# Kernel optimization log

Measured on AMD Instinct MI355X. Metric: run time of the kernel, lower is better.

## Reference

```python
import jax, jax.numpy as jnp
import numpy as np

N, E, IN, HID, OUT = 100000, 1600000, 128, 64, 64
NEG = 0.2   # GATConv negative_slope default
EPS = 1e-5


def _gat(x, src, dst, W, a_s, a_d, b, n):
    # PyG GATConv, heads=1: h = x W; e_ij = LeakyReLU(a_s.h_j + a_d.h_i);
    # softmax over incoming edges of i; out_i = sum_j alpha_ij h_j + b
    h = x @ W                                   # [N, F]
    s = (h @ a_s)[src] + (h @ a_d)[dst]         # [E]
    e = jnp.where(s >= 0, s, NEG * s)
    m = jax.ops.segment_max(e, dst, num_segments=n)
    w = jnp.exp(e - m[dst])
    z = jax.ops.segment_sum(w, dst, num_segments=n)
    alpha = w / z[dst]
    out = jax.ops.segment_sum(h[src] * alpha[:, None], dst, num_segments=n)
    return out + b


def _graph_ln(x, g, b):
    # PyG LayerNorm mode='graph' (default): normalize over all nodes+features
    mu = jnp.mean(x)
    var = jnp.mean((x - mu) ** 2)
    return (x - mu) * jax.lax.rsqrt(var + EPS) * g + b


def _prelu(x, a):
    return jnp.where(x >= 0, x, a * x)


def _encoder(x, edge_index, params):
    n = x.shape[0]
    loops = jnp.arange(n, dtype=edge_index.dtype)  # GATConv add_self_loops=True
    src = jnp.concatenate([edge_index[0], loops])
    dst = jnp.concatenate([edge_index[1], loops])
    for (W, a_s, a_d, b, g, be, p) in params:
        x = _gat(x, src, dst, W, a_s, a_d, b, n)
        x = _graph_ln(x, g, be)
        x = _prelu(x, p)
    return x


def setup_inputs():
    key = jax.random.key(0)
    ks = jax.random.split(key, 32)
    d = {}
    d["x_q"] = jax.random.normal(ks[0], (N, IN), jnp.float32)
    d["x_k"] = jax.random.normal(ks[1], (N, IN), jnp.float32)
    d["edge_index_q"] = jax.random.randint(ks[2], (2, E), 0, N)
    d["edge_index_k"] = jax.random.randint(ks[3], (2, E), 0, N)
    i = 4
    for pre, fi, fo in [("q1", IN, HID), ("q2", HID, OUT), ("k1", IN, HID), ("k2", HID, OUT)]:
        d[pre + "_W"] = jax.random.normal(ks[i], (fi, fo), jnp.float32) / np.sqrt(fi).astype(np.float32); i += 1
        d[pre + "_as"] = jax.random.normal(ks[i], (fo,), jnp.float32) * 0.1; i += 1
        d[pre + "_ad"] = jax.random.normal(ks[i], (fo,), jnp.float32) * 0.1; i += 1
        d[pre + "_b"] = jnp.zeros((fo,), jnp.float32)
        d[pre + "_g"] = jnp.ones((fo,), jnp.float32)
        d[pre + "_be"] = jnp.zeros((fo,), jnp.float32)
        d[pre + "_p"] = jnp.full((1,), 0.25, jnp.float32)
    d["m_W1"] = jax.random.normal(ks[i], (OUT, 2 * OUT), jnp.float32) / np.sqrt(OUT).astype(np.float32); i += 1
    d["m_b1"] = jnp.zeros((2 * OUT,), jnp.float32)
    d["m_p"] = jnp.full((1,), 0.25, jnp.float32)
    d["m_W2"] = jax.random.normal(ks[i], (2 * OUT, OUT), jnp.float32) / np.sqrt(2 * OUT).astype(np.float32)
    d["m_b2"] = jnp.zeros((OUT,), jnp.float32)
    return d


def reference(x_q, x_k, edge_index_q, edge_index_k,
              q1_W, q1_as, q1_ad, q1_b, q1_g, q1_be, q1_p,
              q2_W, q2_as, q2_ad, q2_b, q2_g, q2_be, q2_p,
              k1_W, k1_as, k1_ad, k1_b, k1_g, k1_be, k1_p,
              k2_W, k2_as, k2_ad, k2_b, k2_g, k2_be, k2_p,
              m_W1, m_b1, m_p, m_W2, m_b2):
    Q = _encoder(x_q, edge_index_q,
                 [(q1_W, q1_as, q1_ad, q1_b, q1_g, q1_be, q1_p),
                  (q2_W, q2_as, q2_ad, q2_b, q2_g, q2_be, q2_p)])
    Q = _prelu(Q @ m_W1 + m_b1, m_p) @ m_W2 + m_b2
    K = _encoder(x_k, edge_index_k,
                 [(k1_W, k1_as, k1_ad, k1_b, k1_g, k1_be, k1_p),
                  (k2_W, k2_as, k2_ad, k2_b, k2_g, k2_be, k2_p)])
    return (Q, jax.lax.stop_gradient(K))
```

## Files before the change

### kernel.cpp

```cpp
#include <hip/hip_runtime.h>
#include <cstddef>
#include <cstdint>

#define NEG_SLOPE 0.2f
#define LN_EPS    1e-5f
#define NBUK      256
#define MAXNPB    512

typedef unsigned short ushort_t;
typedef short bf16x8 __attribute__((ext_vector_type(8)));
typedef float f32x4  __attribute__((ext_vector_type(4)));

__device__ __forceinline__ float lrelu(float s) { return s >= 0.f ? s : NEG_SLOPE * s; }
__device__ __forceinline__ float b2f(ushort_t u) { return __uint_as_float(((uint32_t)u) << 16); }
__device__ __forceinline__ ushort_t f2b(float f) {
  uint32_t u = __float_as_uint(f);
  return (ushort_t)((u + 0x7fffu + ((u >> 16) & 1u)) >> 16);
}
__device__ __forceinline__ uint2 pack4(float4 v) {
  uint2 r;
  r.x = (uint32_t)f2b(v.x) | ((uint32_t)f2b(v.y) << 16);
  r.y = (uint32_t)f2b(v.z) | ((uint32_t)f2b(v.w) << 16);
  return r;
}


__global__ void kb_init(int* __restrict__ gbcur, int cap) {
  gbcur[threadIdx.x] = threadIdx.x * cap;
}

__global__ __launch_bounds__(256) void kb_expand(const int* __restrict__ src,
                                                 const int* __restrict__ dst, int E,
                                                 int* __restrict__ gbcur,
                                                 int2* __restrict__ pairs, uint32_t bmul) {
  __shared__ int hist[NBUK], base[NBUK], lcnt[NBUK];
  const int tid = threadIdx.x;
  const int nchunk = (E + 4095) >> 12;
  for (int c = blockIdx.x; c < nchunk; c += gridDim.x) {
    const int e0 = c << 12;
    hist[tid] = 0; lcnt[tid] = 0;
    __syncthreads();
    int sv[16], dv[16], bv[16];
    #pragma unroll
    for (int u = 0; u < 16; ++u) {
      const int i = e0 + u * 256 + tid;
      if (i < E) {
        sv[u] = src[i]; dv[u] = dst[i];
        bv[u] = (int)__umulhi((uint32_t)dv[u], bmul);
        atomicAdd(&hist[bv[u]], 1);
      } else bv[u] = -1;
    }
    __syncthreads();
    base[tid] = atomicAdd(&gbcur[tid], hist[tid]);
    __syncthreads();
    #pragma unroll
    for (int u = 0; u < 16; ++u) {
      if (bv[u] >= 0) {
        const int pos = atomicAdd(&lcnt[bv[u]], 1);
        pairs[base[bv[u]] + pos] = make_int2(sv[u], dv[u]);
      }
    }
    __syncthreads();
  }
}

__global__ __launch_bounds__(256) void kb_sort(const int2* __restrict__ pairs,
                                               const int* __restrict__ gbcur,
                                               int* __restrict__ rs, int* __restrict__ re,
                                               int* __restrict__ csr,
                                               uint32_t bmul, int cap, int N) {
  __shared__ int hist[MAXNPB];
  __shared__ int ps[256];
  const int b = blockIdx.x, tid = threadIdx.x;
  int n0 = (int)((((uint64_t)b << 32) + bmul - 1) / bmul);
  int n1 = (int)((((uint64_t)(b + 1) << 32) + bmul - 1) / bmul);
  n0 = n0 < N ? n0 : N;
  n1 = n1 < N ? n1 : N;
  const int nn = n1 - n0;
  const int e0 = b * cap;
  const int e1 = min(gbcur[b], e0 + cap);
  for (int k = tid; k < nn; k += 256) hist[k] = 0;
  __syncthreads();
  for (int i = e0 + tid; i < e1; i += 256) atomicAdd(&hist[pairs[i].y - n0], 1);
  __syncthreads();
  const int i0 = 2 * tid, i1 = 2 * tid + 1;
  const int a = (i0 < nn) ? hist[i0] : 0;
  const int c = (i1 < nn) ? hist[i1] : 0;
  const int tot = a + c;
  ps[tid] = tot;
  __syncthreads();
  for (int off = 1; off < 256; off <<= 1) {
    const int x = (tid >= off) ? ps[tid - off] : 0;
    __syncthreads();
    ps[tid] += x;
    __syncthreads();
  }
  const int excl = ps[tid] - tot;
  if (i0 < nn) { hist[i0] = excl;     rs[n0 + i0] = e0 + excl;     re[n0 + i0] = e0 + excl + a; }
  if (i1 < nn) { hist[i1] = excl + a; rs[n0 + i1] = e0 + excl + a; re[n0 + i1] = e0 + excl + a + c; }
  __syncthreads();
  for (int i = e0 + tid; i < e1; i += 256) {
    const int2 e = pairs[i];
    const int p = atomicAdd(&hist[e.y - n0], 1);
    csr[e0 + p] = e.x;
  }
}

template <int FI, bool LNF>
__global__ __launch_bounds__(256) void k_gemm_att(
    const void* __restrict__ act, int N,
    const float* __restrict__ W, const float* __restrict__ a_s, const float* __restrict__ a_d,
    const float* __restrict__ stats, const float* __restrict__ g,
    const float* __restrict__ be, const float* __restrict__ pp,
    ushort_t* __restrict__ h16, float* __restrict__ hs, float* __restrict__ hd)
{
  constexpr int P = FI + 8;
  __shared__ ushort_t S[64 * P];
  const int tid = threadIdx.x, wid = tid >> 6, lane = tid & 63;
  const int l15 = lane & 15, lhi = lane >> 4;

  for (int idx = tid; idx < FI * 64; idx += 256) {
    const int k = idx >> 6, f = idx & 63;
    S[f * P + k] = f2b(W[idx]);
  }
  __syncthreads();
  bf16x8 Bf[FI / 32][4];
  #pragma unroll
  for (int kt = 0; kt < FI / 32; ++kt)
    #pragma unroll
    for (int nt = 0; nt < 4; ++nt)
      Bf[kt][nt] = *(const bf16x8*)&S[(nt * 16 + l15) * P + kt * 32 + lhi * 8];
  __syncthreads();

  float asf[4], adf[4];
  #pragma unroll
  for (int nt = 0; nt < 4; ++nt) { asf[nt] = a_s[nt * 16 + l15]; adf[nt] = a_d[nt * 16 + l15]; }
  float mu = 0.f, rstd = 1.f, p0 = 0.f;
  if (LNF) { mu = stats[0]; rstd = stats[1]; p0 = pp[0]; }

  const int ntiles = (N + 63) >> 6;
  for (int tile = blockIdx.x; tile < ntiles; tile += gridDim.x) {
    const int nb = tile << 6;
    {
      const int r = tid >> 2;
      const int node = nb + r;
      if (node < N) {
        if (LNF) {
          const ushort_t* a16 = (const ushort_t*)act;
          const int q = tid & 3;
          const int4* srcp = (const int4*)(a16 + (size_t)node * 64 + q * 16);
          const int4 A0 = srcp[0], A1 = srcp[1];
          const ushort_t* pu0 = (const ushort_t*)&A0;
          const ushort_t* pu1 = (const ushort_t*)&A1;
          float vv[16];
          #pragma unroll
          for (int i = 0; i < 8; ++i) { vv[i] = b2f(pu0[i]); vv[8 + i] = b2f(pu1[i]); }
          #pragma unroll
          for (int i2 = 0; i2 < 4; ++i2) {
            const int c4 = q * 4 + i2;
            const float4 gg = ((const float4*)g)[c4];
            const float4 bb = ((const float4*)be)[c4];
            float4 v;
            v.x = (vv[i2 * 4 + 0] - mu) * rstd * gg.x + bb.x;  v.x = v.x >= 0.f ? v.x : p0 * v.x;
            v.y = (vv[i2 * 4 + 1] - mu) * rstd * gg.y + bb.y;  v.y = v.y >= 0.f ? v.y : p0 * v.y;
            v.z = (vv[i2 * 4 + 2] - mu) * rstd * gg.z + bb.z;  v.z = v.z >= 0.f ? v.z : p0 * v.z;
            v.w = (vv[i2 * 4 + 3] - mu) * rstd * gg.w + bb.w;  v.w = v.w >= 0.f ? v.w : p0 * v.w;
            *(uint2*)&S[r * P + c4 * 4] = pack4(v);
          }
        } else {
          const float4* srcp = (const float4*)((const float*)act + (size_t)node * FI);
          #pragma unroll
          for (int i = 0; i < FI / 16; ++i) {
            const int c = (tid & 3) * (FI / 4) + i * 4;
            const float4 v = srcp[c >> 2];
            *(uint2*)&S[r * P + c] = pack4(v);
          }
        }
      }
    }
    __syncthreads();

    const f32x4 fz = {0.f, 0.f, 0.f, 0.f};
    f32x4 acc[4]; acc[0] = fz; acc[1] = fz; acc[2] = fz; acc[3] = fz;
    #pragma unroll
    for (int kt = 0; kt < FI / 32; ++kt) {
      const bf16x8 Af = *(const bf16x8*)&S[(wid * 16 + l15) * P + kt * 32 + lhi * 8];
      #pragma unroll
      for (int nt = 0; nt < 4; ++nt)
        acc[nt] = __builtin_amdgcn_mfma_f32_16x16x32_bf16(Af, Bf[kt][nt], acc[nt], 0, 0, 0);
    }
    #pragma unroll
    for (int r = 0; r < 4; ++r) {
      float ps = acc[0][r] * asf[0] + acc[1][r] * asf[1] + acc[2][r] * asf[2] + acc[3][r] * asf[3];
      float pd = acc[0][r] * adf[0] + acc[1][r] * adf[1] + acc[2][r] * adf[2] + acc[3][r] * adf[3];
      #pragma unroll
      for (int off = 1; off < 16; off <<= 1) { ps += __shfl_xor(ps, off); pd += __shfl_xor(pd, off); }
      const int node = nb + wid * 16 + lhi * 4 + r;
      if (l15 == 0 && node < N) { hs[node] = ps; hd[node] = pd; }
    }
    #pragma unroll
    for (int nt = 0; nt < 4; ++nt)
      #pragma unroll
      for (int r = 0; r < 4; ++r)
        S[(wid * 16 + lhi * 4 + r) * P + nt * 16 + l15] = f2b(acc[nt][r]);
    __syncthreads();
    {
      const int r = tid >> 2, chunk = tid & 3;
      const int node = nb + r;
      if (node < N) {
        const int4* sp = (const int4*)&S[r * P + chunk * 16];
        const int4 v0 = sp[0], v1 = sp[1];
        int4* dp = (int4*)(h16 + (size_t)node * 64 + chunk * 16);
        dp[0] = v0; dp[1] = v1;
      }
    }
    __syncthreads();
  }
}

__global__ __launch_bounds__(256) void k_aggregate(
    const int* __restrict__ rs, const int* __restrict__ re, const int* __restrict__ csr,
    const ushort_t* __restrict__ h16, const float* __restrict__ hs, const float* __restrict__ hd,
    const float* __restrict__ bias, int N,
    ushort_t* __restrict__ y16, float* __restrict__ part)
{
  __shared__ float wsh[4][32];
  __shared__ float sh1[4], sh2[4];
  const int tid = threadIdx.x, wid = tid >> 6, lane = tid & 63;
  const int node = blockIdx.x * 4 + wid;
  float val = 0.f;
  if (node < N) {
    const float hdi = hd[node];
    const float wself = __expf(lrelu(hs[node] + hdi));
    float z = wself;
    float acc0 = wself * b2f(h16[((size_t)(uint32_t)node << 6) + lane]);
    float acc1 = 0.f, acc2 = 0.f, acc3 = 0.f;
    const int st = __builtin_amdgcn_readfirstlane(rs[node]);
    const int en = __builtin_amdgcn_readfirstlane(re[node]);
    for (int j = st; j < en; j += 32) {
      const int m = min(32, en - j);
      int sA = 0;
      if (lane < m) sA = csr[j + lane];
      #define GA(u) h16[((size_t)(uint32_t)__builtin_amdgcn_readlane(sA, u) << 6) + lane]
      ushort_t g0 = 0, g1 = 0, g2 = 0, g3 = 0, g4 = 0, g5 = 0, g6 = 0, g7 = 0;
      ushort_t g8 = 0, g9 = 0, g10 = 0, g11 = 0, g12 = 0, g13 = 0, g14 = 0, g15 = 0;
      ushort_t g16 = 0, g17 = 0, g18 = 0, g19 = 0, g20 = 0, g21 = 0, g22 = 0, g23 = 0;
      ushort_t g24 = 0, g25 = 0, g26 = 0, g27 = 0, g28 = 0, g29 = 0, g30 = 0, g31 = 0;
      if (m > 0)  { g0  = GA(0);  g1  = GA(1);  g2  = GA(2);  g3  = GA(3);  }
      if (m > 4)  { g4  = GA(4);  g5  = GA(5);  g6  = GA(6);  g7  = GA(7);  }
      if (m > 8)  { g8  = GA(8);  g9  = GA(9);  g10 = GA(10); g11 = GA(11); }
      if (m > 12) { g12 = GA(12); g13 = GA(13); g14 = GA(14); g15 = GA(15); }
      if (m > 16) { g16 = GA(16); g17 = GA(17); g18 = GA(18); g19 = GA(19); }
      if (m > 20) { g20 = GA(20); g21 = GA(21); g22 = GA(22); g23 = GA(23); }
      if (m > 24) { g24 = GA(24); g25 = GA(25); g26 = GA(26); g27 = GA(27); }
      if (m > 28) { g28 = GA(28); g29 = GA(29); g30 = GA(30); g31 = GA(31); }
      #undef GA
      float wA = 0.f;
      if (lane < m) wA = __expf(lrelu(hs[sA] + hdi));
      if (lane < 32) wsh[wid][lane] = wA;
      float ws = wA;
      #pragma unroll
      for (int off = 32; off; off >>= 1) ws += __shfl_xor(ws, off);
      z += ws;
      #define CS(u, a) a = fmaf(wsh[wid][u], b2f(g##u), a)
      if (m > 0)  { CS(0, acc0);  CS(1, acc1);  CS(2, acc2);  CS(3, acc3);  }
      if (m > 4)  { CS(4, acc0);  CS(5, acc1);  CS(6, acc2);  CS(7, acc3);  }
      if (m > 8)  { CS(8, acc0);  CS(9, acc1);  CS(10, acc2); CS(11, acc3); }
      if (m > 12) { CS(12, acc0); CS(13, acc1); CS(14, acc2); CS(15, acc3); }
      if (m > 16) { CS(16, acc0); CS(17, acc1); CS(18, acc2); CS(19, acc3); }
      if (m > 20) { CS(20, acc0); CS(21, acc1); CS(22, acc2); CS(23, acc3); }
      if (m > 24) { CS(24, acc0); CS(25, acc1); CS(26, acc2); CS(27, acc3); }
      if (m > 28) { CS(28, acc0); CS(29, acc1); CS(30, acc2); CS(31, acc3); }
      #undef CS
    }
    val = ((acc0 + acc1) + (acc2 + acc3)) / z + bias[lane];
    y16[(size_t)node * 64 + lane] = f2b(val);
  }
  float s1r = val, s2r = val * val;
  #pragma unroll
  for (int off = 32; off; off >>= 1) { s1r += __shfl_xor(s1r, off); s2r += __shfl_xor(s2r, off); }
  if (lane == 0) { sh1[wid] = s1r; sh2[wid] = s2r; }
  __syncthreads();
  if (tid == 0) {
    part[(size_t)blockIdx.x * 2 + 0] = sh1[0] + sh1[1] + sh1[2] + sh1[3];
    part[(size_t)blockIdx.x * 2 + 1] = sh2[0] + sh2[1] + sh2[2] + sh2[3];
  }
}

__global__ __launch_bounds__(1024) void k_ln_stats(
    const float* __restrict__ part, int nblk, float invCount, float* __restrict__ statsOut)
{
  __shared__ float sh1[16], sh2[16];
  float s1 = 0.f, s2 = 0.f;
  for (int i = threadIdx.x; i < nblk; i += 1024) { s1 += part[(size_t)i * 2]; s2 += part[(size_t)i * 2 + 1]; }
  #pragma unroll
  for (int off = 32; off; off >>= 1) { s1 += __shfl_xor(s1, off); s2 += __shfl_xor(s2, off); }
  const int wid = threadIdx.x >> 6, lane = threadIdx.x & 63;
  if (lane == 0) { sh1[wid] = s1; sh2[wid] = s2; }
  __syncthreads();
  if (threadIdx.x == 0) {
    float t1 = 0.f, t2 = 0.f;
    #pragma unroll
    for (int i = 0; i < 16; ++i) { t1 += sh1[i]; t2 += sh2[i]; }
    const float mu = t1 * invCount;
    const float var = t2 * invCount - mu * mu;
    statsOut[0] = mu;
    statsOut[1] = rsqrtf(var + LN_EPS);
  }
}

__global__ __launch_bounds__(256) void k_mlp(
    const ushort_t* __restrict__ y16, int N,
    const float* __restrict__ stats, const float* __restrict__ g,
    const float* __restrict__ be, const float* __restrict__ pe,
    const float* __restrict__ W1, const float* __restrict__ b1, const float* __restrict__ pm,
    const float* __restrict__ W2, const float* __restrict__ b2,
    float* __restrict__ outp)
{
  __shared__ ushort_t W1t[128 * 72];
  __shared__ ushort_t W2t[64 * 136];
  __shared__ ushort_t At[64 * 72];
  __shared__ ushort_t Tt[64 * 136];
  __shared__ float    Ob[64 * 68];
  const int tid = threadIdx.x, wid = tid >> 6, lane = tid & 63;
  const int l15 = lane & 15, lhi = lane >> 4;

  for (int idx = tid; idx < 64 * 128; idx += 256) {
    const int k = idx >> 7, f = idx & 127;
    W1t[f * 72 + k] = f2b(W1[idx]);
  }
  for (int idx = tid; idx < 128 * 64; idx += 256) {
    const int k = idx >> 6, f = idx & 63;
    W2t[f * 136 + k] = f2b(W2[idx]);
  }
  __syncthreads();

  const float mu = stats[0], rstd = stats[1], p0 = pe[0], pm0 = pm[0];
  float b1f[8], b2f_[4];
  #pragma unroll
  for (int nt = 0; nt < 8; ++nt) b1f[nt] = b1[nt * 16 + l15];
  #pragma unroll
  for (int nt = 0; nt < 4; ++nt) b2f_[nt] = b2[nt * 16 + l15];

  const int ntiles = (N + 63) >> 6;
  for (int tile = blockIdx.x; tile < ntiles; tile += gridDim.x) {
    const int nb = tile << 6;
    {
      const int r = tid >> 2;
      const int node = nb + r;
      if (node < N) {
        const int q = tid & 3;
        const int4* srcp = (const int4*)(y16 + (size_t)node * 64 + q * 16);
        const int4 A0 = srcp[0], A1 = srcp[1];
        const ushort_t* pu0 = (const ushort_t*)&A0;
        const ushort_t* pu1 = (const ushort_t*)&A1;
        float vv[16];
        #pragma unroll
        for (int i = 0; i < 8; ++i) { vv[i] = b2f(pu0[i]); vv[8 + i] = b2f(pu1[i]); }
        #pragma unroll
        for (int i2 = 0; i2 < 4; ++i2) {
          const int c4 = q * 4 + i2;
          const float4 gg = ((const float4*)g)[c4];
          const float4 bb = ((const float4*)be)[c4];
          float4 v;
          v.x = (vv[i2 * 4 + 0] - mu) * rstd * gg.x + bb.x;  v.x = v.x >= 0.f ? v.x : p0 * v.x;
          v.y = (vv[i2 * 4 + 1] - mu) * rstd * gg.y + bb.y;  v.y = v.y >= 0.f ? v.y : p0 * v.y;
          v.z = (vv[i2 * 4 + 2] - mu) * rstd * gg.z + bb.z;  v.z = v.z >= 0.f ? v.z : p0 * v.z;
          v.w = (vv[i2 * 4 + 3] - mu) * rstd * gg.w + bb.w;  v.w = v.w >= 0.f ? v.w : p0 * v.w;
          *(uint2*)&At[r * 72 + c4 * 4] = pack4(v);
        }
      }
    }
    __syncthreads();

    const f32x4 fz = {0.f, 0.f, 0.f, 0.f};
    f32x4 acc1[8];
    #pragma unroll
    for (int nt = 0; nt < 8; ++nt) acc1[nt] = fz;
    #pragma unroll
    for (int kt = 0; kt < 2; ++kt) {
      const bf16x8 Af = *(const bf16x8*)&At[(wid * 16 + l15) * 72 + kt * 32 + lhi * 8];
      #pragma unroll
      for (int nt = 0; nt < 8; ++nt) {
        const bf16x8 Bf = *(const bf16x8*)&W1t[(nt * 16 + l15) * 72 + kt * 32 + lhi * 8];
        acc1[nt] = __builtin_amdgcn_mfma_f32_16x16x32_bf16(Af, Bf, acc1[nt], 0, 0, 0);
      }
    }
    #pragma unroll
    for (int nt = 0; nt < 8; ++nt)
      #pragma unroll
      for (int r = 0; r < 4; ++r) {
        float v = acc1[nt][r] + b1f[nt];
        v = v >= 0.f ? v : pm0 * v;
        Tt[(wid * 16 + lhi * 4 + r) * 136 + nt * 16 + l15] = f2b(v);
      }
    __syncthreads();

    f32x4 acc2[4];
    #pragma unroll
    for (int nt = 0; nt < 4; ++nt) acc2[nt] = fz;
    #pragma unroll
    for (int kt = 0; kt < 4; ++kt) {
      const bf16x8 Af = *(const bf16x8*)&Tt[(wid * 16 + l15) * 136 + kt * 32 + lhi * 8];
      #pragma unroll
      for (int nt = 0; nt < 4; ++nt) {
        const bf16x8 Bf = *(const bf16x8*)&W2t[(nt * 16 + l15) * 136 + kt * 32 + lhi * 8];
        acc2[nt] = __builtin_amdgcn_mfma_f32_16x16x32_bf16(Af, Bf, acc2[nt], 0, 0, 0);
      }
    }
    #pragma unroll
    for (int nt = 0; nt < 4; ++nt)
      #pragma unroll
      for (int r = 0; r < 4; ++r)
        Ob[(wid * 16 + lhi * 4 + r) * 68 + nt * 16 + l15] = acc2[nt][r] + b2f_[nt];
    __syncthreads();
    {
      const int r = tid >> 2, chunk = tid & 3;
      const int node = nb + r;
      if (node < N) {
        const float4* sp = (const float4*)&Ob[r * 68 + chunk * 16];
        const float4 v0 = sp[0], v1 = sp[1], v2 = sp[2], v3 = sp[3];
        float4* dp = (float4*)(outp + (size_t)node * 64 + chunk * 16);
        dp[0] = v0; dp[1] = v1; dp[2] = v2; dp[3] = v3;
      }
    }
    __syncthreads();
  }
}

__global__ void k_ln_prelu_out(const ushort_t* __restrict__ y16, int total8,
                               const float* __restrict__ stats, const float* __restrict__ g,
                               const float* __restrict__ be, const float* __restrict__ pe,
                               float* __restrict__ o)
{
  const float mu = stats[0], rstd = stats[1], p0 = pe[0];
  int i = blockIdx.x * blockDim.x + threadIdx.x;
  const int stride = gridDim.x * blockDim.x;
  for (; i < total8; i += stride) {
    const int4 A = *(const int4*)(y16 + (size_t)i * 8);
    const ushort_t* pu = (const ushort_t*)&A;
    const int grp = i & 7;
    const float4 g0 = ((const float4*)g)[grp * 2], g1 = ((const float4*)g)[grp * 2 + 1];
    const float4 b0 = ((const float4*)be)[grp * 2], b1 = ((const float4*)be)[grp * 2 + 1];
    float4 o0, o1;
    o0.x = (b2f(pu[0]) - mu) * rstd * g0.x + b0.x;  o0.x = o0.x >= 0.f ? o0.x : p0 * o0.x;
    o0.y = (b2f(pu[1]) - mu) * rstd * g0.y + b0.y;  o0.y = o0.y >= 0.f ? o0.y : p0 * o0.y;
    o0.z = (b2f(pu[2]) - mu) * rstd * g0.z + b0.z;  o0.z = o0.z >= 0.f ? o0.z : p0 * o0.z;
    o0.w = (b2f(pu[3]) - mu) * rstd * g0.w + b0.w;  o0.w = o0.w >= 0.f ? o0.w : p0 * o0.w;
    o1.x = (b2f(pu[4]) - mu) * rstd * g1.x + b1.x;  o1.x = o1.x >= 0.f ? o1.x : p0 * o1.x;
    o1.y = (b2f(pu[5]) - mu) * rstd * g1.y + b1.y;  o1.y = o1.y >= 0.f ? o1.y : p0 * o1.y;
    o1.z = (b2f(pu[6]) - mu) * rstd * g1.z + b1.z;  o1.z = o1.z >= 0.f ? o1.z : p0 * o1.z;
    o1.w = (b2f(pu[7]) - mu) * rstd * g1.w + b1.w;  o1.w = o1.w >= 0.f ? o1.w : p0 * o1.w;
    float4* dp = (float4*)(o + (size_t)i * 8);
    dp[0] = o0; dp[1] = o1;
  }
}

extern "C" void kernel_launch(void* const* d_in, const int* in_sizes, int n_in,
                              void* d_out, int out_size, void* d_ws, size_t ws_size,
                              hipStream_t stream) {
  (void)n_in; (void)out_size; (void)ws_size;
  const int FIN = 128, F = 64;
  const int N = in_sizes[0] / FIN;
  const int E = in_sizes[2] / 2;

  const float* x_q = (const float*)d_in[0];
  const float* x_k = (const float*)d_in[1];
  const int*   ei_q = (const int*)d_in[2];
  const int*   ei_k = (const int*)d_in[3];
  const float* L[4][7];
  for (int l = 0; l < 4; ++l)
    for (int j = 0; j < 7; ++j) L[l][j] = (const float*)d_in[4 + l * 7 + j];
  const float* mW1 = (const float*)d_in[32];
  const float* mb1 = (const float*)d_in[33];
  const float* mp  = (const float*)d_in[34];
  const float* mW2 = (const float*)d_in[35];
  const float* mb2 = (const float*)d_in[36];
  float* out = (float*)d_out;

  const int CAP = (((E + NBUK - 1) / NBUK) * 3 / 2 + 3) & ~3;

  char* w = (char*)d_ws;
  auto alloc = [&](size_t bytes) { char* r = w; w += (bytes + 255) & ~size_t(255); return r; };
  ushort_t* h16 = (ushort_t*)alloc((size_t)N * F * sizeof(ushort_t));
  ushort_t* y16 = (ushort_t*)alloc((size_t)N * F * sizeof(ushort_t));
  float* hs    = (float*)alloc((size_t)N * sizeof(float));
  float* hd    = (float*)alloc((size_t)N * sizeof(float));
  const int nblk = (N + 3) / 4;
  float* part  = (float*)alloc((size_t)nblk * 2 * sizeof(float));
  float* stats = (float*)alloc(16 * sizeof(float));
  int* rs      = (int*)alloc((size_t)N * sizeof(int));
  int* re      = (int*)alloc((size_t)N * sizeof(int));
  int* csr     = (int*)alloc((size_t)NBUK * CAP * sizeof(int));
  int* bcur    = (int*)alloc(NBUK * sizeof(int));
  int2* pairs  = (int2*)alloc((size_t)NBUK * CAP * sizeof(int2));

  const float invCount = 1.f / ((float)N * (float)F);
  const uint32_t bmul = (uint32_t)(((uint64_t)NBUK << 32) / (uint64_t)N);

  auto build_csr = [&](const int* ei) {
    kb_init<<<1, NBUK, 0, stream>>>(bcur, CAP);
    kb_expand<<<512, 256, 0, stream>>>(ei, ei + E, E, bcur, pairs, bmul);
    kb_sort<<<NBUK, 256, 0, stream>>>(pairs, bcur, rs, re, csr, bmul, CAP, N);
  };

  auto run_layers = [&](const float* x0, int li0) {
    const float* const* A = L[li0];
    k_gemm_att<128, false><<<512, 256, 0, stream>>>(
        x0, N, A[0], A[1], A[2], nullptr, nullptr, nullptr, nullptr, h16, hs, hd);
    k_aggregate<<<nblk, 256, 0, stream>>>(rs, re, csr, h16, hs, hd, A[3], N, y16, part);
    k_ln_stats<<<1, 1024, 0, stream>>>(part, nblk, invCount, stats + 2 * li0);
    const float* const* B = L[li0 + 1];
    k_gemm_att<64, true><<<512, 256, 0, stream>>>(
        y16, N, B[0], B[1], B[2], stats + 2 * li0, A[4], A[5], A[6], h16, hs, hd);
    k_aggregate<<<nblk, 256, 0, stream>>>(rs, re, csr, h16, hs, hd, B[3], N, y16, part);
    k_ln_stats<<<1, 1024, 0, stream>>>(part, nblk, invCount, stats + 2 * (li0 + 1));
  };

  build_csr(ei_q);
  run_layers(x_q, 0);
  k_mlp<<<512, 256, 0, stream>>>(y16, N, stats + 2, L[1][4], L[1][5], L[1][6],
                                 mW1, mb1, mp, mW2, mb2, out);

  build_csr(ei_k);
  run_layers(x_k, 2);
  const int total8 = N * F / 8;
  k_ln_prelu_out<<<2048, 256, 0, stream>>>(y16, total8, stats + 6,
                                           L[3][4], L[3][5], L[3][6],
                                           out + (size_t)N * F);
}
```

Baseline: 453.7 us.

## Batch query and key encoder stages into shared dual-path kernel launches

```diff
diff --git a/kernel.cpp b/kernel.cpp
--- a/kernel.cpp
+++ b/kernel.cpp
@@ -24,54 +24,67 @@
   return r;
 }
 
-
-__global__ void kb_init(int* __restrict__ gbcur, int cap) {
-  gbcur[threadIdx.x] = threadIdx.x * cap;
-}
-
-__global__ __launch_bounds__(256) void kb_expand(const int* __restrict__ src,
-                                                 const int* __restrict__ dst, int E,
-                                                 int* __restrict__ gbcur,
-                                                 int2* __restrict__ pairs, uint32_t bmul) {
+__global__ void kb_init(int* __restrict__ b0, int* __restrict__ b1, int cap) {
+  b0[threadIdx.x] = threadIdx.x * cap;
+  b1[threadIdx.x] = threadIdx.x * cap;
+}
+
+__global__ __launch_bounds__(256) void kb_expand(
+    const int* __restrict__ ei0, const int* __restrict__ ei1, int E, int nchunk,
+    int* __restrict__ bcur0, int* __restrict__ bcur1,
+    int2* __restrict__ pairs0, int2* __restrict__ pairs1, uint32_t bmul) {
   __shared__ int hist[NBUK], base[NBUK], lcnt[NBUK];
   const int tid = threadIdx.x;
-  const int nchunk = (E + 4095) >> 12;
-  for (int c = blockIdx.x; c < nchunk; c += gridDim.x) {
-    const int e0 = c << 12;
-    hist[tid] = 0; lcnt[tid] = 0;
-    __syncthreads();
-    int sv[16], dv[16], bv[16];
-    #pragma unroll
-    for (int u = 0; u < 16; ++u) {
-      const int i = e0 + u * 256 + tid;
-      if (i < E) {
-        sv[u] = src[i]; dv[u] = dst[i];
-        bv[u] = (int)__umulhi((uint32_t)dv[u], bmul);
-        atomicAdd(&hist[bv[u]], 1);
-      } else bv[u] = -1;
-    }
-    __syncthreads();
-    base[tid] = atomicAdd(&gbcur[tid], hist[tid]);
-    __syncthreads();
-    #pragma unroll
-    for (int u = 0; u < 16; ++u) {
-      if (bv[u] >= 0) {
-        const int pos = atomicAdd(&lcnt[bv[u]], 1);
-        pairs[base[bv[u]] + pos] = make_int2(sv[u], dv[u]);
-      }
-    }
-    __syncthreads();
-  }
-}
-
-__global__ __launch_bounds__(256) void kb_sort(const int2* __restrict__ pairs,
-                                               const int* __restrict__ gbcur,
-                                               int* __restrict__ rs, int* __restrict__ re,
-                                               int* __restrict__ csr,
-                                               uint32_t bmul, int cap, int N) {
+  const int path = (blockIdx.x >= (unsigned)nchunk) ? 1 : 0;
+  const int c = blockIdx.x - path * nchunk;
+  const int* src = path ? ei1 : ei0;
+  const int* dst = src + E;
+  int* gbcur = path ? bcur1 : bcur0;
+  int2* pairs = path ? pairs1 : pairs0;
+
+  const int e0 = c << 12;
+  hist[tid] = 0; lcnt[tid] = 0;
+  __syncthreads();
+  int sv[16], dv[16], bv[16];
+  #pragma unroll
+  for (int u = 0; u < 16; ++u) {
+    const int i = e0 + u * 256 + tid;
+    if (i < E) {
+      sv[u] = src[i]; dv[u] = dst[i];
+      bv[u] = (int)__umulhi((uint32_t)dv[u], bmul);
+      atomicAdd(&hist[bv[u]], 1);
+    } else bv[u] = -1;
+  }
+  __syncthreads();
+  base[tid] = atomicAdd(&gbcur[tid], hist[tid]);
+  __syncthreads();
+  #pragma unroll
+  for (int u = 0; u < 16; ++u) {
+    if (bv[u] >= 0) {
+      const int pos = atomicAdd(&lcnt[bv[u]], 1);
+      pairs[base[bv[u]] + pos] = make_int2(sv[u], dv[u]);
+    }
+  }
+}
+
+__global__ __launch_bounds__(256) void kb_sort(
+    const int2* __restrict__ pairs0, const int2* __restrict__ pairs1,
+    const int* __restrict__ bcur0, const int* __restrict__ bcur1,
+    int* __restrict__ rs0, int* __restrict__ rs1,
+    int* __restrict__ re0, int* __restrict__ re1,
+    int* __restrict__ csr0, int* __restrict__ csr1,
+    uint32_t bmul, int cap, int N) {
   __shared__ int hist[MAXNPB];
   __shared__ int ps[256];
-  const int b = blockIdx.x, tid = threadIdx.x;
+  const int path = (blockIdx.x >= NBUK) ? 1 : 0;
+  const int b = blockIdx.x & (NBUK - 1);
+  const int tid = threadIdx.x;
+  const int2* pairs = path ? pairs1 : pairs0;
+  const int* gbcur = path ? bcur1 : bcur0;
+  int* rs = path ? rs1 : rs0;
+  int* re = path ? re1 : re0;
+  int* csr = path ? csr1 : csr0;
+
   int n0 = (int)((((uint64_t)b << 32) + bmul - 1) / bmul);
   int n1 = (int)((((uint64_t)(b + 1) << 32) + bmul - 1) / bmul);
   n0 = n0 < N ? n0 : N;
@@ -108,17 +121,37 @@
 
 template <int FI, bool LNF>
 __global__ __launch_bounds__(256) void k_gemm_att(
-    const void* __restrict__ act, int N,
-    const float* __restrict__ W, const float* __restrict__ a_s, const float* __restrict__ a_d,
-    const float* __restrict__ stats, const float* __restrict__ g,
-    const float* __restrict__ be, const float* __restrict__ pp,
-    ushort_t* __restrict__ h16, float* __restrict__ hs, float* __restrict__ hd)
+    const void* __restrict__ act0, const void* __restrict__ act1, int N, int ntiles,
+    const float* __restrict__ W0, const float* __restrict__ W1x,
+    const float* __restrict__ as0, const float* __restrict__ as1,
+    const float* __restrict__ ad0, const float* __restrict__ ad1,
+    const float* __restrict__ st0, const float* __restrict__ st1,
+    const float* __restrict__ g0, const float* __restrict__ g1,
+    const float* __restrict__ be0, const float* __restrict__ be1,
+    const float* __restrict__ pp0, const float* __restrict__ pp1,
+    ushort_t* __restrict__ h0, ushort_t* __restrict__ h1,
+    float* __restrict__ hs0, float* __restrict__ hs1,
+    float* __restrict__ hd0, float* __restrict__ hd1)
 {
   constexpr int P = FI + 8;
   __shared__ ushort_t S[64 * P];
   const int tid = threadIdx.x, wid = tid >> 6, lane = tid & 63;
   const int l15 = lane & 15, lhi = lane >> 4;
 
+  const int path = (blockIdx.x >= (unsigned)ntiles) ? 1 : 0;
+  const int tile = blockIdx.x - path * ntiles;
+  const void* act = path ? act1 : act0;
+  const float* W  = path ? W1x : W0;
+  const float* a_s = path ? as1 : as0;
+  const float* a_d = path ? ad1 : ad0;
+  const float* stats = path ? st1 : st0;
+  const float* g  = path ? g1 : g0;
+  const float* be = path ? be1 : be0;
+  const float* pp = path ? pp1 : pp0;
+  ushort_t* h16 = path ? h1 : h0;
+  float* hs = path ? hs1 : hs0;
+  float* hd = path ? hd1 : hd0;
+
   for (int idx = tid; idx < FI * 64; idx += 256) {
     const int k = idx >> 6, f = idx & 63;
     S[f * P + k] = f2b(W[idx]);
@@ -138,96 +171,110 @@
   float mu = 0.f, rstd = 1.f, p0 = 0.f;
   if (LNF) { mu = stats[0]; rstd = stats[1]; p0 = pp[0]; }
 
-  const int ntiles = (N + 63) >> 6;
-  for (int tile = blockIdx.x; tile < ntiles; tile += gridDim.x) {
-    const int nb = tile << 6;
-    {
-      const int r = tid >> 2;
-      const int node = nb + r;
-      if (node < N) {
-        if (LNF) {
-          const ushort_t* a16 = (const ushort_t*)act;
-          const int q = tid & 3;
-          const int4* srcp = (const int4*)(a16 + (size_t)node * 64 + q * 16);
-          const int4 A0 = srcp[0], A1 = srcp[1];
-          const ushort_t* pu0 = (const ushort_t*)&A0;
-          const ushort_t* pu1 = (const ushort_t*)&A1;
-          float vv[16];
-          #pragma unroll
-          for (int i = 0; i < 8; ++i) { vv[i] = b2f(pu0[i]); vv[8 + i] = b2f(pu1[i]); }
-          #pragma unroll
-          for (int i2 = 0; i2 < 4; ++i2) {
-            const int c4 = q * 4 + i2;
-            const float4 gg = ((const float4*)g)[c4];
-            const float4 bb = ((const float4*)be)[c4];
-            float4 v;
-            v.x = (vv[i2 * 4 + 0] - mu) * rstd * gg.x + bb.x;  v.x = v.x >= 0.f ? v.x : p0 * v.x;
-            v.y = (vv[i2 * 4 + 1] - mu) * rstd * gg.y + bb.y;  v.y = v.y >= 0.f ? v.y : p0 * v.y;
-            v.z = (vv[i2 * 4 + 2] - mu) * rstd * gg.z + bb.z;  v.z = v.z >= 0.f ? v.z : p0 * v.z;
-            v.w = (vv[i2 * 4 + 3] - mu) * rstd * gg.w + bb.w;  v.w = v.w >= 0.f ? v.w : p0 * v.w;
-            *(uint2*)&S[r * P + c4 * 4] = pack4(v);
-          }
-        } else {
-          const float4* srcp = (const float4*)((const float*)act + (size_t)node * FI);
-          #pragma unroll
-          for (int i = 0; i < FI / 16; ++i) {
-            const int c = (tid & 3) * (FI / 4) + i * 4;
-            const float4 v = srcp[c >> 2];
-            *(uint2*)&S[r * P + c] = pack4(v);
-          }
+  const int nb = tile << 6;
+  {
+    const int r = tid >> 2;
+    const int node = nb + r;
+    if (node < N) {
+      if (LNF) {
+        const ushort_t* a16 = (const ushort_t*)act;
+        const int q = tid & 3;
+        const int4* srcp = (const int4*)(a16 + (size_t)node * 64 + q * 16);
+        const int4 A0 = srcp[0], A1 = srcp[1];
+        const ushort_t* pu0 = (const ushort_t*)&A0;
+        const ushort_t* pu1 = (const ushort_t*)&A1;
+        float vv[16];
+        #pragma unroll
+        for (int i = 0; i < 8; ++i) { vv[i] = b2f(pu0[i]); vv[8 + i] = b2f(pu1[i]); }
+        #pragma unroll
+        for (int i2 = 0; i2 < 4; ++i2) {
+          const int c4 = q * 4 + i2;
+          const float4 gg = ((const float4*)g)[c4];
+          const float4 bb = ((const float4*)be)[c4];
+          float4 v;
+          v.x = (vv[i2 * 4 + 0] - mu) * rstd * gg.x + bb.x;  v.x = v.x >= 0.f ? v.x : p0 * v.x;
+          v.y = (vv[i2 * 4 + 1] - mu) * rstd * gg.y + bb.y;  v.y = v.y >= 0.f ? v.y : p0 * v.y;
+          v.z = (vv[i2 * 4 + 2] - mu) * rstd * gg.z + bb.z;  v.z = v.z >= 0.f ? v.z : p0 * v.z;
+          v.w = (vv[i2 * 4 + 3] - mu) * rstd * gg.w + bb.w;  v.w = v.w >= 0.f ? v.w : p0 * v.w;
+          *(uint2*)&S[r * P + c4 * 4] = pack4(v);
+        }
+      } else {
+        const float4* srcp = (const float4*)((const float*)act + (size_t)node * FI);
+        #pragma unroll
+        for (int i = 0; i < FI / 16; ++i) {
+          const int c = (tid & 3) * (FI / 4) + i * 4;
+          const float4 v = srcp[c >> 2];
+          *(uint2*)&S[r * P + c] = pack4(v);
         }
       }
     }
-    __syncthreads();
-
-    const f32x4 fz = {0.f, 0.f, 0.f, 0.f};
-    f32x4 acc[4]; acc[0] = fz; acc[1] = fz; acc[2] = fz; acc[3] = fz;
-    #pragma unroll
-    for (int kt = 0; kt < FI / 32; ++kt) {
-      const bf16x8 Af = *(const bf16x8*)&S[(wid * 16 + l15) * P + kt * 32 + lhi * 8];
-      #pragma unroll
-      for (int nt = 0; nt < 4; ++nt)
-        acc[nt] = __builtin_amdgcn_mfma_f32_16x16x32_bf16(Af, Bf[kt][nt], acc[nt], 0, 0, 0);
-    }
-    #pragma unroll
-    for (int r = 0; r < 4; ++r) {
-      float ps = acc[0][r] * asf[0] + acc[1][r] * asf[1] + acc[2][r] * asf[2] + acc[3][r] * asf[3];
-      float pd = acc[0][r] * adf[0] + acc[1][r] * adf[1] + acc[2][r] * adf[2] + acc[3][r] * adf[3];
-      #pragma unroll
-      for (int off = 1; off < 16; off <<= 1) { ps += __shfl_xor(ps, off); pd += __shfl_xor(pd, off); }
-      const int node = nb + wid * 16 + lhi * 4 + r;
-      if (l15 == 0 && node < N) { hs[node] = ps; hd[node] = pd; }
-    }
+  }
+  __syncthreads();
+
+  const f32x4 fz = {0.f, 0.f, 0.f, 0.f};
+  f32x4 acc[4]; acc[0] = fz; acc[1] = fz; acc[2] = fz; acc[3] = fz;
+  #pragma unroll
+  for (int kt = 0; kt < FI / 32; ++kt) {
+    const bf16x8 Af = *(const bf16x8*)&S[(wid * 16 + l15) * P + kt * 32 + lhi * 8];
     #pragma unroll
     for (int nt = 0; nt < 4; ++nt)
-      #pragma unroll
-      for (int r = 0; r < 4; ++r)
-        S[(wid * 16 + lhi * 4 + r) * P + nt * 16 + l15] = f2b(acc[nt][r]);
-    __syncthreads();
-    {
-      const int r = tid >> 2, chunk = tid & 3;
-      const int node = nb + r;
-      if (node < N) {
-        const int4* sp = (const int4*)&S[r * P + chunk * 16];
-        const int4 v0 = sp[0], v1 = sp[1];
-        int4* dp = (int4*)(h16 + (size_t)node * 64 + chunk * 16);
-        dp[0] = v0; dp[1] = v1;
-      }
-    }
-    __syncthreads();
+      acc[nt] = __builtin_amdgcn_mfma_f32_16x16x32_bf16(Af, Bf[kt][nt], acc[nt], 0, 0, 0);
+  }
+  #pragma unroll
+  for (int r = 0; r < 4; ++r) {
+    float ps = acc[0][r] * asf[0] + acc[1][r] * asf[1] + acc[2][r] * asf[2] + acc[3][r] * asf[3];
+    float pd = acc[0][r] * adf[0] + acc[1][r] * adf[1] + acc[2][r] * adf[2] + acc[3][r] * adf[3];
+    #pragma unroll
+    for (int off = 1; off < 16; off <<= 1) { ps += __shfl_xor(ps, off); pd += __shfl_xor(pd, off); }
+    const int node = nb + wid * 16 + lhi * 4 + r;
+    if (l15 == 0 && node < N) { hs[node] = ps; hd[node] = pd; }
+  }
+  #pragma unroll
+  for (int nt = 0; nt < 4; ++nt)
+    #pragma unroll
+    for (int r = 0; r < 4; ++r)
+      S[(wid * 16 + lhi * 4 + r) * P + nt * 16 + l15] = f2b(acc[nt][r]);
+  __syncthreads();
+  {
+    const int r = tid >> 2, chunk = tid & 3;
+    const int node = nb + r;
+    if (node < N) {
+      const int4* sp = (const int4*)&S[r * P + chunk * 16];
+      const int4 v0 = sp[0], v1 = sp[1];
+      int4* dp = (int4*)(h16 + (size_t)node * 64 + chunk * 16);
+      dp[0] = v0; dp[1] = v1;
+    }
   }
 }
 
 __global__ __launch_bounds__(256) void k_aggregate(
-    const int* __restrict__ rs, const int* __restrict__ re, const int* __restrict__ csr,
-    const ushort_t* __restrict__ h16, const float* __restrict__ hs, const float* __restrict__ hd,
-    const float* __restrict__ bias, int N,
-    ushort_t* __restrict__ y16, float* __restrict__ part)
+    const int* __restrict__ rs0, const int* __restrict__ rs1,
+    const int* __restrict__ re0, const int* __restrict__ re1,
+    const int* __restrict__ csr0, const int* __restrict__ csr1,
+    const ushort_t* __restrict__ h0, const ushort_t* __restrict__ h1,
+    const float* __restrict__ hs0, const float* __restrict__ hs1,
+    const float* __restrict__ hd0, const float* __restrict__ hd1,
+    const float* __restrict__ bias0, const float* __restrict__ bias1,
+    int N, int nblk,
+    ushort_t* __restrict__ y0, ushort_t* __restrict__ y1,
+    float* __restrict__ part0, float* __restrict__ part1)
 {
   __shared__ float wsh[4][32];
   __shared__ float sh1[4], sh2[4];
   const int tid = threadIdx.x, wid = tid >> 6, lane = tid & 63;
-  const int node = blockIdx.x * 4 + wid;
+  const int path = (blockIdx.x >= (unsigned)nblk) ? 1 : 0;
+  const int bb = blockIdx.x - path * nblk;
+  const int* rs = path ? rs1 : rs0;
+  const int* re = path ? re1 : re0;
+  const int* csr = path ? csr1 : csr0;
+  const ushort_t* h16 = path ? h1 : h0;
+  const float* hs = path ? hs1 : hs0;
+  const float* hd = path ? hd1 : hd0;
+  const float* bias = path ? bias1 : bias0;
+  ushort_t* y16 = path ? y1 : y0;
+  float* part = path ? part1 : part0;
+
+  const int node = bb * 4 + wid;
   float val = 0.f;
   if (node < N) {
     const float hdi = hd[node];
@@ -282,30 +329,33 @@
   if (lane == 0) { sh1[wid] = s1r; sh2[wid] = s2r; }
   __syncthreads();
   if (tid == 0) {
-    part[(size_t)blockIdx.x * 2 + 0] = sh1[0] + sh1[1] + sh1[2] + sh1[3];
-    part[(size_t)blockIdx.x * 2 + 1] = sh2[0] + sh2[1] + sh2[2] + sh2[3];
+    part[(size_t)bb * 2 + 0] = sh1[0] + sh1[1] + sh1[2] + sh1[3];
+    part[(size_t)bb * 2 + 1] = sh2[0] + sh2[1] + sh2[2] + sh2[3];
   }
 }
 
 __global__ __launch_bounds__(1024) void k_ln_stats(
-    const float* __restrict__ part, int nblk, float invCount, float* __restrict__ statsOut)
+    const float* __restrict__ part0, const float* __restrict__ part1,
+    int nblk, float invCount,
+    float* __restrict__ s0, float* __restrict__ s1)
 {
   __shared__ float sh1[16], sh2[16];
-  float s1 = 0.f, s2 = 0.f;
-  for (int i = threadIdx.x; i < nblk; i += 1024) { s1 += part[(size_t)i * 2]; s2 += part[(size_t)i * 2 + 1]; }
-  #pragma unroll
-  for (int off = 32; off; off >>= 1) { s1 += __shfl_xor(s1, off); s2 += __shfl_xor(s2, off); }
+  const float* part = blockIdx.x ? part1 : part0;
+  float* so = blockIdx.x ? s1 : s0;
+  float a = 0.f, b = 0.f;
+  for (int i = threadIdx.x; i < nblk; i += 1024) { a += part[(size_t)i * 2]; b += part[(size_t)i * 2 + 1]; }
+  #pragma unroll
+  for (int off = 32; off; off >>= 1) { a += __shfl_xor(a, off); b += __shfl_xor(b, off); }
   const int wid = threadIdx.x >> 6, lane = threadIdx.x & 63;
-  if (lane == 0) { sh1[wid] = s1; sh2[wid] = s2; }
+  if (lane == 0) { sh1[wid] = a; sh2[wid] = b; }
   __syncthreads();
   if (threadIdx.x == 0) {
     float t1 = 0.f, t2 = 0.f;
     #pragma unroll
     for (int i = 0; i < 16; ++i) { t1 += sh1[i]; t2 += sh2[i]; }
     const float mu = t1 * invCount;
-    const float var = t2 * invCount - mu * mu;
-    statsOut[0] = mu;
-    statsOut[1] = rsqrtf(var + LN_EPS);
+    so[0] = mu;
+    so[1] = rsqrtf(t2 * invCount - mu * mu + LN_EPS);
   }
 }
 
@@ -335,105 +385,104 @@
   }
   __syncthreads();
 
-  const float mu = stats[0], rstd = stats[1], p0 = pe[0], pm0 = pm[0];
+  const float mu = stats[0], rstd = stats[1];
+  const float p0 = pe[0], pm0 = pm[0];
   float b1f[8], b2f_[4];
   #pragma unroll
   for (int nt = 0; nt < 8; ++nt) b1f[nt] = b1[nt * 16 + l15];
   #pragma unroll
   for (int nt = 0; nt < 4; ++nt) b2f_[nt] = b2[nt * 16 + l15];
 
-  const int ntiles = (N + 63) >> 6;
-  for (int tile = blockIdx.x; tile < ntiles; tile += gridDim.x) {
-    const int nb = tile << 6;
-    {
-      const int r = tid >> 2;
-      const int node = nb + r;
-      if (node < N) {
-        const int q = tid & 3;
-        const int4* srcp = (const int4*)(y16 + (size_t)node * 64 + q * 16);
-        const int4 A0 = srcp[0], A1 = srcp[1];
-        const ushort_t* pu0 = (const ushort_t*)&A0;
-        const ushort_t* pu1 = (const ushort_t*)&A1;
-        float vv[16];
-        #pragma unroll
-        for (int i = 0; i < 8; ++i) { vv[i] = b2f(pu0[i]); vv[8 + i] = b2f(pu1[i]); }
-        #pragma unroll
-        for (int i2 = 0; i2 < 4; ++i2) {
-          const int c4 = q * 4 + i2;
-          const float4 gg = ((const float4*)g)[c4];
-          const float4 bb = ((const float4*)be)[c4];
-          float4 v;
-          v.x = (vv[i2 * 4 + 0] - mu) * rstd * gg.x + bb.x;  v.x = v.x >= 0.f ? v.x : p0 * v.x;
-          v.y = (vv[i2 * 4 + 1] - mu) * rstd * gg.y + bb.y;  v.y = v.y >= 0.f ? v.y : p0 * v.y;
-          v.z = (vv[i2 * 4 + 2] - mu) * rstd * gg.z + bb.z;  v.z = v.z >= 0.f ? v.z : p0 * v.z;
-          v.w = (vv[i2 * 4 + 3] - mu) * rstd * gg.w + bb.w;  v.w = v.w >= 0.f ? v.w : p0 * v.w;
-          *(uint2*)&At[r * 72 + c4 * 4] = pack4(v);
-        }
+  const int nb = blockIdx.x << 6;
+  {
+    const int r = tid >> 2;
+    const int node = nb + r;
+    if (node < N) {
+      const int q = tid & 3;
+      const int4* srcp = (const int4*)(y16 + (size_t)node * 64 + q * 16);
+      const int4 A0 = srcp[0], A1 = srcp[1];
+      const ushort_t* pu0 = (const ushort_t*)&A0;
+      const ushort_t* pu1 = (const ushort_t*)&A1;
+      float vv[16];
+      #pragma unroll
+      for (int i = 0; i < 8; ++i) { vv[i] = b2f(pu0[i]); vv[8 + i] = b2f(pu1[i]); }
+      #pragma unroll
+      for (int i2 = 0; i2 < 4; ++i2) {
+        const int c4 = q * 4 + i2;
+        const float4 gg = ((const float4*)g)[c4];
+        const float4 bb = ((const float4*)be)[c4];
+        float4 v;
+        v.x = (vv[i2 * 4 + 0] - mu) * rstd * gg.x + bb.x;  v.x = v.x >= 0.f ? v.x : p0 * v.x;
+        v.y = (vv[i2 * 4 + 1] - mu) * rstd * gg.y + bb.y;  v.y = v.y >= 0.f ? v.y : p0 * v.y;
+        v.z = (vv[i2 * 4 + 2] - mu) * rstd * gg.z + bb.z;  v.z = v.z >= 0.f ? v.z : p0 * v.z;
+        v.w = (vv[i2 * 4 + 3] - mu) * rstd * gg.w + bb.w;  v.w = v.w >= 0.f ? v.w : p0 * v.w;
+        *(uint2*)&At[r * 72 + c4 * 4] = pack4(v);
       }
     }
-    __syncthreads();
-
-    const f32x4 fz = {0.f, 0.f, 0.f, 0.f};
-    f32x4 acc1[8];
-    #pragma unroll
-    for (int nt = 0; nt < 8; ++nt) acc1[nt] = fz;
-    #pragma unroll
-    for (int kt = 0; kt < 2; ++kt) {
-      const bf16x8 Af = *(const bf16x8*)&At[(wid * 16 + l15) * 72 + kt * 32 + lhi * 8];
-      #pragma unroll
-      for (int nt = 0; nt < 8; ++nt) {
-        const bf16x8 Bf = *(const bf16x8*)&W1t[(nt * 16 + l15) * 72 + kt * 32 + lhi * 8];
-        acc1[nt] = __builtin_amdgcn_mfma_f32_16x16x32_bf16(Af, Bf, acc1[nt], 0, 0, 0);
-      }
-    }
-    #pragma unroll
-    for (int nt = 0; nt < 8; ++nt)
-      #pragma unroll
-      for (int r = 0; r < 4; ++r) {
-        float v = acc1[nt][r] + b1f[nt];
-        v = v >= 0.f ? v : pm0 * v;
-        Tt[(wid * 16 + lhi * 4 + r) * 136 + nt * 16 + l15] = f2b(v);
-      }
-    __syncthreads();
-
-    f32x4 acc2[4];
-    #pragma unroll
-    for (int nt = 0; nt < 4; ++nt) acc2[nt] = fz;
-    #pragma unroll
-    for (int kt = 0; kt < 4; ++kt) {
-      const bf16x8 Af = *(const bf16x8*)&Tt[(wid * 16 + l15) * 136 + kt * 32 + lhi * 8];
-      #pragma unroll
-      for (int nt = 0; nt < 4; ++nt) {
-        const bf16x8 Bf = *(const bf16x8*)&W2t[(nt * 16 + l15) * 136 + kt * 32 + lhi * 8];
-        acc2[nt] = __builtin_amdgcn_mfma_f32_16x16x32_bf16(Af, Bf, acc2[nt], 0, 0, 0);
-      }
-    }
-    #pragma unroll
-    for (int nt = 0; nt < 4; ++nt)
-      #pragma unroll
-      for (int r = 0; r < 4; ++r)
-        Ob[(wid * 16 + lhi * 4 + r) * 68 + nt * 16 + l15] = acc2[nt][r] + b2f_[nt];
-    __syncthreads();
-    {
-      const int r = tid >> 2, chunk = tid & 3;
-      const int node = nb + r;
-      if (node < N) {
-        const float4* sp = (const float4*)&Ob[r * 68 + chunk * 16];
-        const float4 v0 = sp[0], v1 = sp[1], v2 = sp[2], v3 = sp[3];
-        float4* dp = (float4*)(outp + (size_t)node * 64 + chunk * 16);
-        dp[0] = v0; dp[1] = v1; dp[2] = v2; dp[3] = v3;
-      }
-    }
-    __syncthreads();
+  }
+  __syncthreads();
+
+  const f32x4 fz = {0.f, 0.f, 0.f, 0.f};
+  f32x4 acc1[8];
+  #pragma unroll
+  for (int nt = 0; nt < 8; ++nt) acc1[nt] = fz;
+  #pragma unroll
+  for (int kt = 0; kt < 2; ++kt) {
+    const bf16x8 Af = *(const bf16x8*)&At[(wid * 16 + l15) * 72 + kt * 32 + lhi * 8];
+    #pragma unroll
+    for (int nt = 0; nt < 8; ++nt) {
+      const bf16x8 Bf = *(const bf16x8*)&W1t[(nt * 16 + l15) * 72 + kt * 32 + lhi * 8];
+      acc1[nt] = __builtin_amdgcn_mfma_f32_16x16x32_bf16(Af, Bf, acc1[nt], 0, 0, 0);
+    }
+  }
+  #pragma unroll
+  for (int nt = 0; nt < 8; ++nt)
+    #pragma unroll
+    for (int r = 0; r < 4; ++r) {
+      float v = acc1[nt][r] + b1f[nt];
+      v = v >= 0.f ? v : pm0 * v;
+      Tt[(wid * 16 + lhi * 4 + r) * 136 + nt * 16 + l15] = f2b(v);
+    }
+  __syncthreads();
+
+  f32x4 acc2[4];
+  #pragma unroll
+  for (int nt = 0; nt < 4; ++nt) acc2[nt] = fz;
+  #pragma unroll
+  for (int kt = 0; kt < 4; ++kt) {
+    const bf16x8 Af = *(const bf16x8*)&Tt[(wid * 16 + l15) * 136 + kt * 32 + lhi * 8];
+    #pragma unroll
+    for (int nt = 0; nt < 4; ++nt) {
+      const bf16x8 Bf = *(const bf16x8*)&W2t[(nt * 16 + l15) * 136 + kt * 32 + lhi * 8];
+      acc2[nt] = __builtin_amdgcn_mfma_f32_16x16x32_bf16(Af, Bf, acc2[nt], 0, 0, 0);
+    }
+  }
+  #pragma unroll
+  for (int nt = 0; nt < 4; ++nt)
+    #pragma unroll
+    for (int r = 0; r < 4; ++r)
+      Ob[(wid * 16 + lhi * 4 + r) * 68 + nt * 16 + l15] = acc2[nt][r] + b2f_[nt];
+  __syncthreads();
+  {
+    const int r = tid >> 2, chunk = tid & 3;
+    const int node = nb + r;
+    if (node < N) {
+      const float4* sp = (const float4*)&Ob[r * 68 + chunk * 16];
+      const float4 v0 = sp[0], v1 = sp[1], v2 = sp[2], v3 = sp[3];
+      float4* dp = (float4*)(outp + (size_t)node * 64 + chunk * 16);
+      dp[0] = v0; dp[1] = v1; dp[2] = v2; dp[3] = v3;
+    }
   }
 }
 
 __global__ void k_ln_prelu_out(const ushort_t* __restrict__ y16, int total8,
-                               const float* __restrict__ stats, const float* __restrict__ g,
+                               const float* __restrict__ stats,
+                               const float* __restrict__ g,
                                const float* __restrict__ be, const float* __restrict__ pe,
                                float* __restrict__ o)
 {
-  const float mu = stats[0], rstd = stats[1], p0 = pe[0];
+  const float mu = stats[0], rstd = stats[1];
+  const float p0 = pe[0];
   int i = blockIdx.x * blockDim.x + threadIdx.x;
   const int stride = gridDim.x * blockDim.x;
   for (; i < total8; i += stride) {
@@ -478,54 +527,68 @@
   const float* mb2 = (const float*)d_in[36];
   float* out = (float*)d_out;
 
-  const int CAP = (((E + NBUK - 1) / NBUK) * 3 / 2 + 3) & ~3;
+  const int CAP = (((E + NBUK - 1) / NBUK) * 5 / 4 + 3) & ~3;
 
   char* w = (char*)d_ws;
   auto alloc = [&](size_t bytes) { char* r = w; w += (bytes + 255) & ~size_t(255); return r; };
-  ushort_t* h16 = (ushort_t*)alloc((size_t)N * F * sizeof(ushort_t));
-  ushort_t* y16 = (ushort_t*)alloc((size_t)N * F * sizeof(ushort_t));
-  float* hs    = (float*)alloc((size_t)N * sizeof(float));
-  float* hd    = (float*)alloc((size_t)N * sizeof(float));
+  ushort_t* h16_0 = (ushort_t*)alloc((size_t)N * F * sizeof(ushort_t));
+  ushort_t* h16_1 = (ushort_t*)alloc((size_t)N * F * sizeof(ushort_t));
+  ushort_t* y16_0 = (ushort_t*)alloc((size_t)N * F * sizeof(ushort_t));
+  ushort_t* y16_1 = (ushort_t*)alloc((size_t)N * F * sizeof(ushort_t));
+  int2* pairs0 = (int2*)h16_0;
+  int2* pairs1 = pairs0 + (size_t)NBUK * CAP;
+  float* hs0 = (float*)alloc((size_t)N * sizeof(float));
+  float* hs1 = (float*)alloc((size_t)N * sizeof(float));
+  float* hd0 = (float*)alloc((size_t)N * sizeof(float));
+  float* hd1 = (float*)alloc((size_t)N * sizeof(float));
   const int nblk = (N + 3) / 4;
-  float* part  = (float*)alloc((size_t)nblk * 2 * sizeof(float));
+  float* part0 = (float*)alloc((size_t)nblk * 2 * sizeof(float));
+  float* part1 = (float*)alloc((size_t)nblk * 2 * sizeof(float));
   float* stats = (float*)alloc(16 * sizeof(float));
-  int* rs      = (int*)alloc((size_t)N * sizeof(int));
-  int* re      = (int*)alloc((size_t)N * sizeof(int));
-  int* csr     = (int*)alloc((size_t)NBUK * CAP * sizeof(int));
-  int* bcur    = (int*)alloc(NBUK * sizeof(int));
-  int2* pairs  = (int2*)alloc((size_t)NBUK * CAP * sizeof(int2));
+  int* rs0 = (int*)alloc((size_t)N * sizeof(int));
+  int* rs1 = (int*)alloc((size_t)N * sizeof(int));
+  int* re0 = (int*)alloc((size_t)N * sizeof(int));
+  int* re1 = (int*)alloc((size_t)N * sizeof(int));
+  int* csr0 = (int*)alloc((size_t)NBUK * CAP * sizeof(int));
+  int* csr1 = (int*)alloc((size_t)NBUK * CAP * sizeof(int));
+  int* bcur0 = (int*)alloc(NBUK * sizeof(int));
+  int* bcur1 = (int*)alloc(NBUK * sizeof(int));
 
   const float invCount = 1.f / ((float)N * (float)F);
   const uint32_t bmul = (uint32_t)(((uint64_t)NBUK << 32) / (uint64_t)N);
-
-  auto build_csr = [&](const int* ei) {
-    kb_init<<<1, NBUK, 0, stream>>>(bcur, CAP);
-    kb_expand<<<512, 256, 0, stream>>>(ei, ei + E, E, bcur, pairs, bmul);
-    kb_sort<<<NBUK, 256, 0, stream>>>(pairs, bcur, rs, re, csr, bmul, CAP, N);
-  };
-
-  auto run_layers = [&](const float* x0, int li0) {
-    const float* const* A = L[li0];
-    k_gemm_att<128, false><<<512, 256, 0, stream>>>(
-        x0, N, A[0], A[1], A[2], nullptr, nullptr, nullptr, nullptr, h16, hs, hd);
-    k_aggregate<<<nblk, 256, 0, stream>>>(rs, re, csr, h16, hs, hd, A[3], N, y16, part);
-    k_ln_stats<<<1, 1024, 0, stream>>>(part, nblk, invCount, stats + 2 * li0);
-    const float* const* B = L[li0 + 1];
-    k_gemm_att<64, true><<<512, 256, 0, stream>>>(
-        y16, N, B[0], B[1], B[2], stats + 2 * li0, A[4], A[5], A[6], h16, hs, hd);
-    k_aggregate<<<nblk, 256, 0, stream>>>(rs, re, csr, h16, hs, hd, B[3], N, y16, part);
-    k_ln_stats<<<1, 1024, 0, stream>>>(part, nblk, invCount, stats + 2 * (li0 + 1));
-  };
-
-  build_csr(ei_q);
-  run_layers(x_q, 0);
-  k_mlp<<<512, 256, 0, stream>>>(y16, N, stats + 2, L[1][4], L[1][5], L[1][6],
-                                 mW1, mb1, mp, mW2, mb2, out);
-
-  build_csr(ei_k);
-  run_layers(x_k, 2);
+  const int ntiles = (N + 63) / 64;
+  const int nchunkE = (E + 4095) >> 12;
+
+  kb_init<<<1, NBUK, 0, stream>>>(bcur0, bcur1, CAP);
+  kb_expand<<<2 * nchunkE, 256, 0, stream>>>(ei_q, ei_k, E, nchunkE,
+                                             bcur0, bcur1, pairs0, pairs1, bmul);
+  kb_sort<<<2 * NBUK, 256, 0, stream>>>(pairs0, pairs1, bcur0, bcur1,
+                                        rs0, rs1, re0, re1, csr0, csr1, bmul, CAP, N);
+
+  k_gemm_att<128, false><<<2 * ntiles, 256, 0, stream>>>(
+      x_q, x_k, N, ntiles,
+      L[0][0], L[2][0], L[0][1], L[2][1], L[0][2], L[2][2],
+      nullptr, nullptr, nullptr, nullptr, nullptr, nullptr, nullptr, nullptr,
+      h16_0, h16_1, hs0, hs1, hd0, hd1);
+  k_aggregate<<<2 * nblk, 256, 0, stream>>>(
+      rs0, rs1, re0, re1, csr0, csr1, h16_0, h16_1, hs0, hs1, hd0, hd1,
+      L[0][3], L[2][3], N, nblk, y16_0, y16_1, part0, part1);
+  k_ln_stats<<<2, 1024, 0, stream>>>(part0, part1, nblk, invCount, stats + 0, stats + 4);
+
+  k_gemm_att<64, true><<<2 * ntiles, 256, 0, stream>>>(
+      y16_0, y16_1, N, ntiles,
+      L[1][0], L[3][0], L[1][1], L[3][1], L[1][2], L[3][2],
+      stats + 0, stats + 4, L[0][4], L[2][4], L[0][5], L[2][5], L[0][6], L[2][6],
+      h16_0, h16_1, hs0, hs1, hd0, hd1);
+  k_aggregate<<<2 * nblk, 256, 0, stream>>>(
+      rs0, rs1, re0, re1, csr0, csr1, h16_0, h16_1, hs0, hs1, hd0, hd1,
+      L[1][3], L[3][3], N, nblk, y16_0, y16_1, part0, part1);
+  k_ln_stats<<<2, 1024, 0, stream>>>(part0, part1, nblk, invCount, stats + 2, stats + 6);
+
+  k_mlp<<<ntiles, 256, 0, stream>>>(y16_0, N, stats + 2, L[1][4], L[1][5], L[1][6],
+                                    mW1, mb1, mp, mW2, mb2, out);
   const int total8 = N * F / 8;
-  k_ln_prelu_out<<<2048, 256, 0, stream>>>(y16, total8, stats + 6,
+  k_ln_prelu_out<<<2048, 256, 0, stream>>>(y16_1, total8, stats + 6,
                                            L[3][4], L[3][5], L[3][6],
                                            out + (size_t)N * F);
 }
```

Result: faster. 398.9 us (-12.1%).
